# Kernel tuning notes

Hardware: AMD Instinct MI355X
Metric: run time of the kernel (lower is better)

Reference implementation:

```python
import jax, jax.numpy as jnp
import numpy as np
from jax import lax

K = 3       # kernel_size
G = 2       # group
STRIDE = 2
BN_EPS = 1e-5


def setup_inputs() -> dict:
    key = jax.random.key(0)
    k1, k2, k3, k4, k5, k6 = jax.random.split(key, 6)
    n, c, h, w = 16, 64, 128, 128
    gk2 = G * K * K
    x = jax.random.normal(k1, (n, c, h, w), dtype=jnp.float32)
    # kaiming_normal_(fan_out) std = sqrt(2 / (out_ch * k * k))
    std = float(np.sqrt(2.0 / (gk2 * K * K)))
    conv_w = jax.random.normal(k2, (gk2, c, K, K), dtype=jnp.float32) * std
    bn_gamma = jax.random.uniform(k3, (gk2,), dtype=jnp.float32, minval=0.5, maxval=1.5)
    bn_beta = jax.random.normal(k4, (gk2,), dtype=jnp.float32) * 0.1
    bn_mean = jax.random.normal(k5, (gk2,), dtype=jnp.float32) * 0.1
    bn_var = jax.random.uniform(k6, (gk2,), dtype=jnp.float32, minval=0.5, maxval=1.5)
    return {"x": x, "conv_w": conv_w, "bn_gamma": bn_gamma, "bn_beta": bn_beta,
            "bn_mean": bn_mean, "bn_var": bn_var}


def _pasa(x, conv_w, bn_gamma, bn_beta, bn_mean, bn_var):
    n, c, h, w = x.shape
    p = K // 2
    xp = jnp.pad(x, ((0, 0), (0, 0), (p, p), (p, p)), mode="reflect")
    # attention logits: conv over padded input, 'VALID' -> same h, w
    sigma = lax.conv_general_dilated(
        xp, conv_w, window_strides=(1, 1), padding="VALID",
        dimension_numbers=("NCHW", "OIHW", "NCHW"))
    # BatchNorm (inference) folded into scale/shift
    inv = bn_gamma * lax.rsqrt(bn_var + BN_EPS)
    sigma = sigma * inv[None, :, None, None] + (bn_beta - bn_mean * inv)[None, :, None, None]
    # softmax over the full g*k*k channel dim (as in the original Softmax(dim=1))
    sigma = jax.nn.softmax(sigma, axis=1)            # [n, g*k*k, h, w]
    sigma = sigma.reshape(n, G, K * K, h, w)
    # im2col: gather k*k shifted views of the padded input -> [n, c, k*k, h, w]
    patches = jnp.stack(
        [xp[:, :, i:i + h, j:j + w] for i in range(K) for j in range(K)], axis=2)
    patches = patches.reshape(n, G, c // G, K * K, h, w)
    # softmax-weighted aggregation over the kernel window
    out = jnp.einsum("ngckhw,ngkhw->ngchw", patches, sigma).reshape(n, c, h, w)
    return out[:, :, ::STRIDE, ::STRIDE]


def reference(x, conv_w, bn_gamma, bn_beta, bn_mean, bn_var):
    return _pasa(x, conv_w, bn_gamma, bn_beta, bn_mean, bn_var)
```

## Files before the change

### kernel.cpp

```cpp
#include <hip/hip_runtime.h>

#define N_  16
#define C_  64
#define H_  128
#define W_  128
#define HO_ 64
#define WO_ 64
#define CO_ 18
#define NSP 8
#define CPS (C_/NSP)

__global__ __launch_bounds__(512, 8)
void pasa_fused2(const float* __restrict__ x,
                 const float* __restrict__ cw,
                 const float* __restrict__ gamma,
                 const float* __restrict__ beta,
                 const float* __restrict__ mean,
                 const float* __restrict__ var,
                 float* __restrict__ out)
{
    __shared__ float part[NSP][CO_][WO_];

    const int tid = threadIdx.x;
    const int wo  = tid & 63;
    const int sp  = tid >> 6;
    const int ho  = blockIdx.x;
    const int n   = blockIdx.y;

    int r0 = 2*ho - 1; if (r0 < 0) r0 = 1;
    const int r1 = 2*ho, r2 = 2*ho + 1;
    const int c1 = 2*wo, c2 = c1 + 1;
    int c0 = c1 - 1; if (c0 < 0) c0 = 1;
    (void)c2;

    const float* __restrict__ xn = x + (size_t)n * (C_*H_*W_);

    float sig[CO_];
#pragma unroll
    for (int o = 0; o < CO_; ++o) sig[o] = 0.f;

#pragma unroll 2
    for (int j = 0; j < CPS; ++j) {
        const int c = __builtin_amdgcn_readfirstlane(sp * CPS + j);
        const float* __restrict__ xc = xn + c * (H_*W_);
        const float  w0  = xc[r0*W_ + c0];
        const float2 w12 = *(const float2*)(xc + r0*W_ + c1);
        const float  w3  = xc[r1*W_ + c0];
        const float2 w45 = *(const float2*)(xc + r1*W_ + c1);
        const float  w6  = xc[r2*W_ + c0];
        const float2 w78 = *(const float2*)(xc + r2*W_ + c1);
        const float* __restrict__ wc = cw + c * 9;
#pragma unroll
        for (int o = 0; o < CO_; ++o) {
            const float* __restrict__ q = wc + o * 576;
            float a = sig[o];
            a = fmaf(w0,    q[0], a);
            a = fmaf(w12.x, q[1], a);
            a = fmaf(w12.y, q[2], a);
            a = fmaf(w3,    q[3], a);
            a = fmaf(w45.x, q[4], a);
            a = fmaf(w45.y, q[5], a);
            a = fmaf(w6,    q[6], a);
            a = fmaf(w78.x, q[7], a);
            a = fmaf(w78.y, q[8], a);
            sig[o] = a;
        }
    }

#pragma unroll
    for (int o = 0; o < CO_; ++o) part[sp][o][wo] = sig[o];
    __syncthreads();
    if (sp < 4) {
#pragma unroll
        for (int o = 0; o < CO_; ++o) part[sp][o][wo] += part[sp+4][o][wo];
    }
    __syncthreads();
    if (sp < 2) {
#pragma unroll
        for (int o = 0; o < CO_; ++o) part[sp][o][wo] += part[sp+2][o][wo];
    }
    __syncthreads();
    if (sp == 0) {
#pragma unroll
        for (int o = 0; o < CO_; ++o) part[0][o][wo] += part[1][o][wo];
    }
    __syncthreads();

    float mx = -3.4e38f;
#pragma unroll
    for (int o = 0; o < CO_; ++o) {
        const float inv = gamma[o] * rsqrtf(var[o] + 1e-5f);
        sig[o] = part[0][o][wo] * inv + (beta[o] - mean[o] * inv);
        mx = fmaxf(mx, sig[o]);
    }
    float sum = 0.f;
#pragma unroll
    for (int o = 0; o < CO_; ++o) { sig[o] = __expf(sig[o] - mx); sum += sig[o]; }
    const float rs = 1.f / sum;

    const int g = sp >> 2;
    float p[9];
    if (g == 0) {
#pragma unroll
        for (int k = 0; k < 9; ++k) p[k] = sig[k] * rs;
    } else {
#pragma unroll
        for (int k = 0; k < 9; ++k) p[k] = sig[9 + k] * rs;
    }

#pragma unroll 2
    for (int j = 0; j < CPS; ++j) {
        const int c = __builtin_amdgcn_readfirstlane(sp * CPS + j);
        const float* __restrict__ xc = xn + c * (H_*W_);
        float acc = xc[r0*W_ + c0] * p[0];
        const float2 a12 = *(const float2*)(xc + r0*W_ + c1);
        acc = fmaf(a12.x, p[1], acc);
        acc = fmaf(a12.y, p[2], acc);
        acc = fmaf(xc[r1*W_ + c0], p[3], acc);
        const float2 a45 = *(const float2*)(xc + r1*W_ + c1);
        acc = fmaf(a45.x, p[4], acc);
        acc = fmaf(a45.y, p[5], acc);
        acc = fmaf(xc[r2*W_ + c0], p[6], acc);
        const float2 a78 = *(const float2*)(xc + r2*W_ + c1);
        acc = fmaf(a78.x, p[7], acc);
        acc = fmaf(a78.y, p[8], acc);
        out[(((size_t)n*C_ + c)*HO_ + ho)*WO_ + wo] = acc;
    }
}

extern "C" void kernel_launch(void* const* d_in, const int* in_sizes, int n_in,
                              void* d_out, int out_size, void* d_ws, size_t ws_size,
                              hipStream_t stream) {
    const float* x     = (const float*)d_in[0];
    const float* cw    = (const float*)d_in[1];
    const float* gamma = (const float*)d_in[2];
    const float* beta  = (const float*)d_in[3];
    const float* mean  = (const float*)d_in[4];
    const float* var   = (const float*)d_in[5];
    float* out = (float*)d_out;

    dim3 grid(HO_, N_);
    pasa_fused2<<<grid, 512, 0, stream>>>(x, cw, gamma, beta, mean, var, out);
}
```

Baseline: 49.45 us.

## Cache input window in registers, reuse for aggregation, and swizzle row order

Each thread now loads its 8 channels' 3x3 input windows once into registers and reuses them both for the attention-logit convolution and for the weighted aggregation, instead of reading global memory twice. All loads are issued up front, which gives more memory-level parallelism. The block-to-output-row mapping is swizzled so that concurrently running blocks touch rows spread across the image. The extra 72 live registers per thread are why launch bounds drop from 8 to 4 blocks per CU, which lowers occupancy.

```diff
diff --git a/kernel.cpp b/kernel.cpp
--- a/kernel.cpp
+++ b/kernel.cpp
@@ -10,8 +10,8 @@
 #define NSP 8
 #define CPS (C_/NSP)
 
-__global__ __launch_bounds__(512, 8)
-void pasa_fused2(const float* __restrict__ x,
+__global__ __launch_bounds__(512, 4)
+void pasa_fused3(const float* __restrict__ x,
                  const float* __restrict__ cw,
                  const float* __restrict__ gamma,
                  const float* __restrict__ beta,
@@ -24,45 +24,47 @@
     const int tid = threadIdx.x;
     const int wo  = tid & 63;
     const int sp  = tid >> 6;
-    const int ho  = blockIdx.x;
+    const int bx  = blockIdx.x;
+    const int ho  = ((bx & 7) << 3) | (bx >> 3);
     const int n   = blockIdx.y;
 
     int r0 = 2*ho - 1; if (r0 < 0) r0 = 1;
     const int r1 = 2*ho, r2 = 2*ho + 1;
-    const int c1 = 2*wo, c2 = c1 + 1;
+    const int c1 = 2*wo;
     int c0 = c1 - 1; if (c0 < 0) c0 = 1;
-    (void)c2;
 
     const float* __restrict__ xn = x + (size_t)n * (C_*H_*W_);
+
+    float wv[CPS][9];
+#pragma unroll
+    for (int j = 0; j < CPS; ++j) {
+        const int c = sp * CPS + j;
+        const float* __restrict__ xc = xn + c * (H_*W_);
+        wv[j][0] = xc[r0*W_ + c0];
+        float2 t = *(const float2*)(xc + r0*W_ + c1);
+        wv[j][1] = t.x; wv[j][2] = t.y;
+        wv[j][3] = xc[r1*W_ + c0];
+        t = *(const float2*)(xc + r1*W_ + c1);
+        wv[j][4] = t.x; wv[j][5] = t.y;
+        wv[j][6] = xc[r2*W_ + c0];
+        t = *(const float2*)(xc + r2*W_ + c1);
+        wv[j][7] = t.x; wv[j][8] = t.y;
+    }
 
     float sig[CO_];
 #pragma unroll
     for (int o = 0; o < CO_; ++o) sig[o] = 0.f;
 
-#pragma unroll 2
+#pragma unroll
     for (int j = 0; j < CPS; ++j) {
         const int c = __builtin_amdgcn_readfirstlane(sp * CPS + j);
-        const float* __restrict__ xc = xn + c * (H_*W_);
-        const float  w0  = xc[r0*W_ + c0];
-        const float2 w12 = *(const float2*)(xc + r0*W_ + c1);
-        const float  w3  = xc[r1*W_ + c0];
-        const float2 w45 = *(const float2*)(xc + r1*W_ + c1);
-        const float  w6  = xc[r2*W_ + c0];
-        const float2 w78 = *(const float2*)(xc + r2*W_ + c1);
         const float* __restrict__ wc = cw + c * 9;
 #pragma unroll
         for (int o = 0; o < CO_; ++o) {
             const float* __restrict__ q = wc + o * 576;
             float a = sig[o];
-            a = fmaf(w0,    q[0], a);
-            a = fmaf(w12.x, q[1], a);
-            a = fmaf(w12.y, q[2], a);
-            a = fmaf(w3,    q[3], a);
-            a = fmaf(w45.x, q[4], a);
-            a = fmaf(w45.y, q[5], a);
-            a = fmaf(w6,    q[6], a);
-            a = fmaf(w78.x, q[7], a);
-            a = fmaf(w78.y, q[8], a);
+#pragma unroll
+            for (int k = 0; k < 9; ++k) a = fmaf(wv[j][k], q[k], a);
             sig[o] = a;
         }
     }
@@ -108,22 +110,12 @@
         for (int k = 0; k < 9; ++k) p[k] = sig[9 + k] * rs;
     }
 
-#pragma unroll 2
+#pragma unroll
     for (int j = 0; j < CPS; ++j) {
-        const int c = __builtin_amdgcn_readfirstlane(sp * CPS + j);
-        const float* __restrict__ xc = xn + c * (H_*W_);
-        float acc = xc[r0*W_ + c0] * p[0];
-        const float2 a12 = *(const float2*)(xc + r0*W_ + c1);
-        acc = fmaf(a12.x, p[1], acc);
-        acc = fmaf(a12.y, p[2], acc);
-        acc = fmaf(xc[r1*W_ + c0], p[3], acc);
-        const float2 a45 = *(const float2*)(xc + r1*W_ + c1);
-        acc = fmaf(a45.x, p[4], acc);
-        acc = fmaf(a45.y, p[5], acc);
-        acc = fmaf(xc[r2*W_ + c0], p[6], acc);
-        const float2 a78 = *(const float2*)(xc + r2*W_ + c1);
-        acc = fmaf(a78.x, p[7], acc);
-        acc = fmaf(a78.y, p[8], acc);
+        const int c = sp * CPS + j;
+        float acc = wv[j][0] * p[0];
+#pragma unroll
+        for (int k = 1; k < 9; ++k) acc = fmaf(wv[j][k], p[k], acc);
         out[(((size_t)n*C_ + c)*HO_ + ho)*WO_ + wo] = acc;
     }
 }
@@ -140,5 +132,5 @@
     float* out = (float*)d_out;
 
     dim3 grid(HO_, N_);
-    pasa_fused2<<<grid, 512, 0, stream>>>(x, cw, gamma, beta, mean, var, out);
+    pasa_fused3<<<grid, 512, 0, stream>>>(x, cw, gamma, beta, mean, var, out);
 }
```

Measured after the change: 43.92 us. 11.2% less time.
